# Kernel tuning notes

Hardware: AMD Instinct MI355X
Metric: run time of the kernel (lower is better)

Reference implementation:

```python
import jax, jax.numpy as jnp
import numpy as np

B, S, D = 2, 2048, 1024
H, DK = 16, 64


def setup_inputs() -> dict:
    key = jax.random.key(0)
    ks = jax.random.split(key, 10)
    scale = D ** -0.5
    x = jax.random.normal(ks[0], (B, S, D), dtype=jnp.float32)
    mask = jax.random.randint(ks[1], (B, S), 0, 2) > 0  # True = masked positions
    Wq = jax.random.normal(ks[2], (D, H * DK), dtype=jnp.float32) * scale
    Wk = jax.random.normal(ks[3], (D, H * DK), dtype=jnp.float32) * scale
    Wv = jax.random.normal(ks[4], (D, H * DK), dtype=jnp.float32) * scale
    Wo = jax.random.normal(ks[5], (H * DK, D), dtype=jnp.float32) * scale
    bq = jnp.zeros((H * DK,), jnp.float32)
    bk = jnp.zeros((H * DK,), jnp.float32)
    bv = jnp.zeros((H * DK,), jnp.float32)
    bo = jnp.zeros((D,), jnp.float32)
    return {"x": x, "mask": mask, "Wq": Wq, "bq": bq, "Wk": Wk, "bk": bk,
            "Wv": Wv, "bv": bv, "Wo": Wo, "bo": bo}


def reference(x, mask, Wq, bq, Wk, bk, Wv, bv, Wo, bo):
    b, s, _ = x.shape
    # Linear + activation (dropout is identity at eval)
    q = jax.nn.relu(x @ Wq + bq).reshape(b, s, H, DK)
    k = jax.nn.relu(x @ Wk + bk).reshape(b, s, H, DK)
    v = jax.nn.relu(x @ Wv + bv).reshape(b, s, H, DK)
    # scores: [B, H, Sq, Sk]
    attn = jnp.einsum("bqhd,bkhd->bhqk", q, k) * (DK ** -0.5)
    # NOTE: original uses masked_fill(mask, 1e-9) BEFORE softmax (not -inf)
    attn = jnp.where(mask[:, None, None, :], jnp.float32(1e-9), attn)
    attn = jax.nn.softmax(attn, axis=-1)
    out = jnp.einsum("bhqk,bkhd->bqhd", attn, v).reshape(b, s, H * DK)
    return jax.nn.relu(out @ Wo + bo)
```

## Files before the change

kernel.cpp:

```cpp
#include <hip/hip_runtime.h>
#include <stdint.h>

typedef __attribute__((ext_vector_type(8))) short short8;
typedef __attribute__((ext_vector_type(4))) short short4b;
typedef __attribute__((ext_vector_type(4))) float f32x4;
typedef __attribute__((ext_vector_type(4))) unsigned short ushort4_t;

#define MFMA16(a, b, c) __builtin_amdgcn_mfma_f32_16x16x32_bf16((a), (b), (c), 0, 0, 0)

#if defined(__HIP_DEVICE_COMPILE__)
  #if __has_builtin(__builtin_amdgcn_mfma_f32_16x16x16bf16_1k)
    #define MFMA16K16(a, b, c) __builtin_amdgcn_mfma_f32_16x16x16bf16_1k((a), (b), (c), 0, 0, 0)
  #else
    #define MFMA16K16(a, b, c) __builtin_amdgcn_mfma_f32_16x16x16_bf16((a), (b), (c), 0, 0, 0)
  #endif
#else
  #define MFMA16K16(a, b, c) (c)
#endif

#define SCL_F (0.125f * 1.44269504f)

__device__ __forceinline__ float b2f(unsigned short u) {
    union { unsigned u; float f; } c; c.u = ((unsigned)u) << 16; return c.f;
}
__device__ __forceinline__ unsigned short f2b(float f) {
    union { float f; unsigned u; } c; c.f = f;
    unsigned r = c.u + 0x7FFF + ((c.u >> 16) & 1);
    return (unsigned short)(r >> 16);
}
__device__ __forceinline__ unsigned f_as_u(float f) {
    union { float f; unsigned u; } c; c.f = f; return c.u;
}

__device__ __forceinline__ void g2lds16(const unsigned short* g, unsigned lds_byte_off) {
    __builtin_amdgcn_global_load_lds(
        (const __attribute__((address_space(1))) void*)(uintptr_t)g,
        (__attribute__((address_space(3))) void*)(uintptr_t)lds_byte_off,
        16, 0, 0);
}

__global__ void detect_dtype(const unsigned short* __restrict__ x, int* __restrict__ flag) {
    __shared__ int cnt;
    if (threadIdx.x == 0) cnt = 0;
    __syncthreads();
    int insane = 0;
    #pragma unroll
    for (int j = 0; j < 4; ++j) {
        unsigned short u = x[threadIdx.x * 4 + j];
        int e = (u >> 7) & 0xFF;
        if ((e >= 1 && e <= 90) || e >= 165) insane++;
    }
    atomicAdd(&cnt, insane);
    __syncthreads();
    if (threadIdx.x == 0) *flag = (cnt > 128) ? 1 : 0;
}

__global__ __launch_bounds__(256) void convtrans_k(const void* __restrict__ s0, const void* __restrict__ s1,
                                                   const void* __restrict__ s2, const void* __restrict__ s3,
                                                   const void* __restrict__ b0, const void* __restrict__ b1,
                                                   const void* __restrict__ b2, const void* __restrict__ b3s,
                                                   const void* __restrict__ xsrc,
                                                   unsigned short* __restrict__ xdst,
                                                   unsigned short* __restrict__ dstBase,
                                                   unsigned short* __restrict__ dstB3,
                                                   unsigned short* __restrict__ dstBo,
                                                   const int* __restrict__ flag) {
    const int z = blockIdx.z;
    if (z >= 5) {
        if (!*flag) return;
        const int slice = z - 5;
        const size_t i0 = (size_t)slice * 524288 + (blockIdx.y * 16 + blockIdx.x) * 2048 + threadIdx.x * 8;
        const float* s = (const float*)xsrc;
        float4 f0 = *(const float4*)&s[i0];
        float4 f1 = *(const float4*)&s[i0 + 4];
        unsigned short* t = &xdst[i0];
        t[0] = f2b(f0.x); t[1] = f2b(f0.y); t[2] = f2b(f0.z); t[3] = f2b(f0.w);
        t[4] = f2b(f1.x); t[5] = f2b(f1.y); t[6] = f2b(f1.z); t[7] = f2b(f1.w);
        return;
    }
    if (z == 4) {
        if (blockIdx.y != 0 || blockIdx.x >= 4) return;
        const int w = blockIdx.x;
        const void* src = (w == 0) ? b0 : (w == 1) ? b1 : (w == 2) ? b2 : b3s;
        const float bscl = (w == 0) ? SCL_F : 1.0f;
        #pragma unroll
        for (int j = 0; j < 4; ++j) {
            const int i = threadIdx.x * 4 + j;
            float fv = (*flag) ? ((const float*)src)[i] : b2f(((const unsigned short*)src)[i]);
            unsigned short v = f2b(fv * bscl);
            if (w < 3) dstB3[w * 1024 + i] = v;
            else dstBo[i] = v;
        }
        return;
    }
    __shared__ __align__(16) unsigned short tile[64 * 72];
    const void* src = (z == 0) ? s0 : (z == 1) ? s1 : (z == 2) ? s2 : s3;
    unsigned short* dst = dstBase + (size_t)z * 1024 * 1024;
    const float wscl = (z == 0) ? SCL_F : 1.0f;
    const int tid = threadIdx.x;
    const int r0 = blockIdx.y * 64, c0 = blockIdx.x * 64;
    const int rb = tid >> 3, c = (tid & 7) * 8;
    if (*flag) {
        const float* s = (const float*)src;
        #pragma unroll
        for (int it = 0; it < 2; ++it) {
            int rr = it * 32 + rb;
            float4 f0 = *(const float4*)&s[(size_t)(r0 + rr) * 1024 + c0 + c];
            float4 f1 = *(const float4*)&s[(size_t)(r0 + rr) * 1024 + c0 + c + 4];
            unsigned short* t = &tile[rr * 72 + c];
            t[0] = f2b(f0.x * wscl); t[1] = f2b(f0.y * wscl); t[2] = f2b(f0.z * wscl); t[3] = f2b(f0.w * wscl);
            t[4] = f2b(f1.x * wscl); t[5] = f2b(f1.y * wscl); t[6] = f2b(f1.z * wscl); t[7] = f2b(f1.w * wscl);
        }
    } else if (z == 0) {
        const unsigned short* s = (const unsigned short*)src;
        #pragma unroll
        for (int it = 0; it < 2; ++it) {
            int rr = it * 32 + rb;
            union { short8 v; unsigned short u[8]; } in;
            in.v = *(const short8*)&s[(size_t)(r0 + rr) * 1024 + c0 + c];
            unsigned short* t = &tile[rr * 72 + c];
            #pragma unroll
            for (int j = 0; j < 8; ++j) t[j] = f2b(b2f(in.u[j]) * SCL_F);
        }
    } else {
        const unsigned short* s = (const unsigned short*)src;
        #pragma unroll
        for (int it = 0; it < 2; ++it) {
            int rr = it * 32 + rb;
            *(short8*)&tile[rr * 72 + c] = *(const short8*)&s[(size_t)(r0 + rr) * 1024 + c0 + c];
        }
    }
    __syncthreads();
    #pragma unroll
    for (int it = 0; it < 2; ++it) {
        int n = it * 32 + rb, k8 = c;
        union { short8 s; unsigned short u[8]; } tmp;
        #pragma unroll
        for (int j = 0; j < 8; ++j) tmp.u[j] = tile[(k8 + j) * 72 + n];
        *(short8*)&dst[(size_t)(c0 + n) * 1024 + r0 + k8] = tmp.s;
    }
}

__global__ __launch_bounds__(256) void mask_k(unsigned short* __restrict__ qkv,
                                              const int* __restrict__ mask) {
    const int row = blockIdx.x * 2 + (threadIdx.x >> 7);
    const int col = (threadIdx.x & 127) * 8;
    if (mask[row]) {
        const short8 z = {0, 0, 0, 0, 0, 0, 0, 0};
        *(short8*)&qkv[(size_t)row * 3072 + 1024 + col] = z;
    }
}

__global__ __launch_bounds__(256) void gemm_bias_relu(const unsigned short* __restrict__ A,
                                                      const void* __restrict__ Araw,
                                                      const unsigned short* __restrict__ BT,
                                                      const unsigned short* __restrict__ bias,
                                                      void* __restrict__ C,
                                                      unsigned short* __restrict__ VtG,
                                                      const int* __restrict__ flag,
                                                      int M, int N, int K, int mode) {
    __shared__ __align__(16) unsigned short As[128 * 32];
    __shared__ __align__(16) unsigned short Bs[128 * 32];
    const int tid = threadIdx.x;
    const int wave = tid >> 6, lane = tid & 63;
    const int quad = lane >> 4, l16 = lane & 15;
    const int wm = wave >> 1, wn = wave & 1;
    const int m0 = blockIdx.y * 128, n0 = blockIdx.x * 128;

    const unsigned short* Ause = (Araw != nullptr && *flag == 0) ? (const unsigned short*)Araw : A;

    f32x4 acc[4][4];
    #pragma unroll
    for (int i = 0; i < 4; i++)
        #pragma unroll
        for (int j = 0; j < 4; j++) acc[i][j] = (f32x4){0.f, 0.f, 0.f, 0.f};

    const int srow = wave * 32 + (lane >> 2);
    const int sc8  = (lane & 3) * 8;
    const unsigned short* gA0 = Ause + (size_t)(m0 + srow) * K + sc8;
    const unsigned short* gA1 = gA0 + (size_t)16 * K;
    const unsigned short* gB0 = BT + (size_t)(n0 + srow) * K + sc8;
    const unsigned short* gB1 = gB0 + (size_t)16 * K;
    const unsigned ldsA = (unsigned)(uintptr_t)&As[0] + wave * 2048;
    const unsigned ldsB = (unsigned)(uintptr_t)&Bs[0] + wave * 2048;

    for (int k0 = 0; k0 < K; k0 += 32) {
        __syncthreads();
        g2lds16(gA0 + k0, ldsA);
        g2lds16(gA1 + k0, ldsA + 1024);
        g2lds16(gB0 + k0, ldsB);
        g2lds16(gB1 + k0, ldsB + 1024);
        __syncthreads();
        short8 af[4], bf[4];
        #pragma unroll
        for (int i = 0; i < 4; i++) af[i] = *(const short8*)&As[(wm * 64 + i * 16 + l16) * 32 + quad * 8];
        #pragma unroll
        for (int j = 0; j < 4; j++) bf[j] = *(const short8*)&Bs[(wn * 64 + j * 16 + l16) * 32 + quad * 8];
        #pragma unroll
        for (int i = 0; i < 4; i++)
            #pragma unroll
            for (int j = 0; j < 4; j++)
                acc[i][j] = MFMA16(af[i], bf[j], acc[i][j]);
    }

    if (mode == 2 && n0 >= 2048) {
        #pragma unroll
        for (int j = 0; j < 4; j++) {
            const int col = n0 + wn * 64 + j * 16 + l16;
            const int h  = (col - 2048) >> 6;
            const int dk = (col - 2048) & 63;
            const float bj = b2f(bias[col]);
            #pragma unroll
            for (int i = 0; i < 4; i++) {
                const int rowb = m0 + wm * 64 + i * 16 + quad * 4;
                const int bb = rowb >> 11;
                const int s0 = rowb & 2047;
                ushort4_t w;
                #pragma unroll
                for (int r = 0; r < 4; r++) {
                    float v = acc[i][j][r] + bj;
                    v = v > 0.f ? v : 0.f;
                    w[r] = f2b(v);
                }
                *(ushort4_t*)&VtG[(size_t)((bb * 16 + h) * 64 + dk) * 2048 + s0] = w;
            }
        }
    } else {
        const int f32out = (mode == 1) && (*flag != 0);
        #pragma unroll
        for (int j = 0; j < 4; j++) {
            const int col = n0 + wn * 64 + j * 16 + l16;
            const float bj = b2f(bias[col]);
            #pragma unroll
            for (int i = 0; i < 4; i++) {
                const int rowb = m0 + wm * 64 + i * 16 + quad * 4;
                #pragma unroll
                for (int r = 0; r < 4; r++) {
                    float v = acc[i][j][r] + bj;
                    v = v > 0.f ? v : 0.f;
                    if (f32out) ((float*)C)[(size_t)(rowb + r) * N + col] = v;
                    else ((unsigned short*)C)[(size_t)(rowb + r) * N + col] = f2b(v);
                }
            }
        }
    }
}

__global__ __launch_bounds__(256) void attn_kernel(const unsigned short* __restrict__ qkv,
                                                   const unsigned short* __restrict__ VtG,
                                                   unsigned short* __restrict__ out) {
    __shared__ __align__(16) unsigned short Ks[64 * 72];
    __shared__ __align__(16) unsigned short Vs[64 * 72];

    const int qt = blockIdx.x, bh = blockIdx.y;
    const int b = bh >> 4, h = bh & 15;
    const int tid = threadIdx.x, wave = tid >> 6, lane = tid & 63;
    const int quad = lane >> 4, l16 = lane & 15;

    const int qrowA = qt * 128 + wave * 16 + l16;
    const unsigned short* qpA = qkv + (size_t)(b * 2048 + qrowA) * 3072 + h * 64;
    const unsigned short* qpB = qpA + (size_t)64 * 3072;
    const short8 qa0 = *(const short8*)(qpA + quad * 8);
    const short8 qa1 = *(const short8*)(qpA + 32 + quad * 8);
    const short8 qb0 = *(const short8*)(qpB + quad * 8);
    const short8 qb1 = *(const short8*)(qpB + 32 + quad * 8);

    f32x4 oA[4], oB[4], sumA, sumB;
    #pragma unroll
    for (int n = 0; n < 4; n++) { oA[n] = (f32x4){0.f,0.f,0.f,0.f}; oB[n] = (f32x4){0.f,0.f,0.f,0.f}; }
    sumA = (f32x4){0.f,0.f,0.f,0.f};
    sumB = (f32x4){0.f,0.f,0.f,0.f};

    const short4b ones = { (short)0x3F80, (short)0x3F80, (short)0x3F80, (short)0x3F80 };

    const int srow = tid >> 2;
    const int scol = (tid & 3) * 16;
    const unsigned short* kg = qkv + (size_t)(b * 2048 + srow) * 3072 + 1024 + h * 64 + scol;
    const unsigned short* vg = VtG + (size_t)(bh * 64 + srow) * 2048 + scol;
    const size_t kstep = (size_t)64 * 3072;
    unsigned short* wK = &Ks[srow * 72 + scol];
    unsigned short* wV = &Vs[srow * 72 + scol];

    for (int kt = 0; kt < 32; ++kt) {
        __syncthreads();
        *(short8*)wK       = *(const short8*)(kg + kt * kstep);
        *(short8*)(wK + 8) = *(const short8*)(kg + kt * kstep + 8);
        *(short8*)wV       = *(const short8*)(vg + kt * 64);
        *(short8*)(wV + 8) = *(const short8*)(vg + kt * 64 + 8);
        __syncthreads();

        f32x4 sA[4], sB[4];
        #pragma unroll
        for (int t = 0; t < 4; ++t) {
            const short8 kb0 = *(const short8*)&Ks[(t * 16 + l16) * 72 + quad * 8];
            const short8 kb1 = *(const short8*)&Ks[(t * 16 + l16) * 72 + 32 + quad * 8];
            f32x4 z = (f32x4){0.f, 0.f, 0.f, 0.f};
            sA[t] = MFMA16(kb1, qa1, MFMA16(kb0, qa0, z));
            sB[t] = MFMA16(kb1, qb1, MFMA16(kb0, qb0, z));
        }

        short4b vb[4][4];
        #pragma unroll
        for (int t = 0; t < 4; ++t)
            #pragma unroll
            for (int n = 0; n < 4; ++n)
                vb[t][n] = *(const short4b*)&Vs[(n * 16 + l16) * 72 + t * 16 + quad * 4];

        #pragma unroll
        for (int t = 0; t < 4; ++t) {
            float pA[4], pB[4];
            #pragma unroll
            for (int r = 0; r < 4; ++r) {
                pA[r] = exp2f(sA[t][r]);
                pB[r] = exp2f(sB[t][r]);
            }
            union { unsigned u[2]; short4b s; } fa, fb;
            fa.u[0] = __builtin_amdgcn_perm(f_as_u(pA[1]), f_as_u(pA[0]), 0x07060302u);
            fa.u[1] = __builtin_amdgcn_perm(f_as_u(pA[3]), f_as_u(pA[2]), 0x07060302u);
            fb.u[0] = __builtin_amdgcn_perm(f_as_u(pB[1]), f_as_u(pB[0]), 0x07060302u);
            fb.u[1] = __builtin_amdgcn_perm(f_as_u(pB[3]), f_as_u(pB[2]), 0x07060302u);
            #pragma unroll
            for (int n = 0; n < 4; ++n) {
                oA[n] = MFMA16K16(fa.s, vb[t][n], oA[n]);
                oB[n] = MFMA16K16(fb.s, vb[t][n], oB[n]);
            }
            sumA = MFMA16K16(fa.s, ones, sumA);
            sumB = MFMA16K16(fb.s, ones, sumB);
        }
    }

    float invA[4], invB[4];
    #pragma unroll
    for (int r = 0; r < 4; ++r) { invA[r] = 1.0f / sumA[r]; invB[r] = 1.0f / sumB[r]; }
    #pragma unroll
    for (int n = 0; n < 4; n++)
        #pragma unroll
        for (int r = 0; r < 4; r++) {
            const int row = qt * 128 + wave * 16 + quad * 4 + r;
            out[(size_t)(b * 2048 + row) * 1024 + h * 64 + n * 16 + l16] = f2b(oA[n][r] * invA[r]);
            out[(size_t)(b * 2048 + row + 64) * 1024 + h * 64 + n * 16 + l16] = f2b(oB[n][r] * invB[r]);
        }
}

extern "C" void kernel_launch(void* const* d_in, const int* in_sizes, int n_in,
                              void* d_out, int out_size, void* d_ws, size_t ws_size,
                              hipStream_t stream) {
    const void* x  = d_in[0];
    const int*  mk = (const int*)d_in[1];
    const void* Wq = d_in[2]; const void* bq = d_in[3];
    const void* Wk = d_in[4]; const void* bk = d_in[5];
    const void* Wv = d_in[6]; const void* bv = d_in[7];
    const void* Wo = d_in[8]; const void* bo = d_in[9];

    char* wsb = (char*)d_ws;
    int* flag = (int*)wsb;
    unsigned short* W0 = (unsigned short*)(wsb + 64);

    const size_t M1 = 1024u * 1024u;
    const size_t M4 = 4096u * 1024u;
    unsigned short* xb  = W0;
    unsigned short* WT  = xb + M4;
    unsigned short* WoT = WT + 3 * M1;
    unsigned short* b3  = WoT + M1;
    unsigned short* bob = b3 + 4096;
    unsigned short* qkv = bob + 1024;
    unsigned short* VtG = qkv + (size_t)4096 * 3072;
    unsigned short* abf = xb;

    detect_dtype<<<1, 256, 0, stream>>>((const unsigned short*)x, flag);

    convtrans_k<<<dim3(16, 16, 13), 256, 0, stream>>>(Wq, Wk, Wv, Wo, bq, bk, bv, bo,
                                                      x, xb, WT, b3, bob, flag);

    gemm_bias_relu<<<dim3(24, 32), 256, 0, stream>>>(xb, x, WT, b3, qkv, VtG, flag,
                                                     4096, 3072, 1024, 2);
    mask_k<<<2048, 256, 0, stream>>>(qkv, mk);
    attn_kernel<<<dim3(16, 32), 256, 0, stream>>>(qkv, VtG, abf);
    gemm_bias_relu<<<dim3(8, 32), 256, 0, stream>>>(abf, nullptr, WoT, bob, d_out, VtG, flag,
                                                    4096, 1024, 1024, 1);
}
```

Before: 233.7 us.

## Split attention key range across two blocks and combine partial results

The attention kernel gains a z grid dimension that splits the 2048 keys into two halves. Each block writes unnormalized partial outputs in bf16 plus per-row softmax sums, reusing the free x buffer and the now-unused V columns of qkv. A new combine kernel adds the two partials and divides by the summed denominators. This doubles the number of attention blocks to improve CU occupancy and latency hiding, at the cost of an extra launch, extra memory traffic and bf16 rounding of the unnormalized partials.

```diff
diff --git a/kernel.cpp b/kernel.cpp
--- a/kernel.cpp
+++ b/kernel.cpp
@@ -248,11 +248,13 @@
 
 __global__ __launch_bounds__(256) void attn_kernel(const unsigned short* __restrict__ qkv,
                                                    const unsigned short* __restrict__ VtG,
-                                                   unsigned short* __restrict__ out) {
+                                                   unsigned short* __restrict__ P0,
+                                                   unsigned short* __restrict__ P1,
+                                                   float* __restrict__ S) {
     __shared__ __align__(16) unsigned short Ks[64 * 72];
     __shared__ __align__(16) unsigned short Vs[64 * 72];
 
-    const int qt = blockIdx.x, bh = blockIdx.y;
+    const int qt = blockIdx.x, bh = blockIdx.y, z = blockIdx.z;
     const int b = bh >> 4, h = bh & 15;
     const int tid = threadIdx.x, wave = tid >> 6, lane = tid & 63;
     const int quad = lane >> 4, l16 = lane & 15;
@@ -275,13 +277,13 @@
 
     const int srow = tid >> 2;
     const int scol = (tid & 3) * 16;
-    const unsigned short* kg = qkv + (size_t)(b * 2048 + srow) * 3072 + 1024 + h * 64 + scol;
-    const unsigned short* vg = VtG + (size_t)(bh * 64 + srow) * 2048 + scol;
+    const unsigned short* kg = qkv + (size_t)(b * 2048 + z * 1024 + srow) * 3072 + 1024 + h * 64 + scol;
+    const unsigned short* vg = VtG + (size_t)(bh * 64 + srow) * 2048 + z * 1024 + scol;
     const size_t kstep = (size_t)64 * 3072;
     unsigned short* wK = &Ks[srow * 72 + scol];
     unsigned short* wV = &Vs[srow * 72 + scol];
 
-    for (int kt = 0; kt < 32; ++kt) {
+    for (int kt = 0; kt < 16; ++kt) {
         __syncthreads();
         *(short8*)wK       = *(const short8*)(kg + kt * kstep);
         *(short8*)(wK + 8) = *(const short8*)(kg + kt * kstep + 8);
@@ -294,9 +296,9 @@
         for (int t = 0; t < 4; ++t) {
             const short8 kb0 = *(const short8*)&Ks[(t * 16 + l16) * 72 + quad * 8];
             const short8 kb1 = *(const short8*)&Ks[(t * 16 + l16) * 72 + 32 + quad * 8];
-            f32x4 z = (f32x4){0.f, 0.f, 0.f, 0.f};
-            sA[t] = MFMA16(kb1, qa1, MFMA16(kb0, qa0, z));
-            sB[t] = MFMA16(kb1, qb1, MFMA16(kb0, qb0, z));
+            f32x4 zz = (f32x4){0.f, 0.f, 0.f, 0.f};
+            sA[t] = MFMA16(kb1, qa1, MFMA16(kb0, qa0, zz));
+            sB[t] = MFMA16(kb1, qb1, MFMA16(kb0, qb0, zz));
         }
 
         short4b vb[4][4];
@@ -329,17 +331,45 @@
         }
     }
 
-    float invA[4], invB[4];
-    #pragma unroll
-    for (int r = 0; r < 4; ++r) { invA[r] = 1.0f / sumA[r]; invB[r] = 1.0f / sumB[r]; }
+    unsigned short* pbase = z ? P1 : P0;
+    const int pstr = z ? 3072 : 1024;
     #pragma unroll
     for (int n = 0; n < 4; n++)
         #pragma unroll
         for (int r = 0; r < 4; r++) {
             const int row = qt * 128 + wave * 16 + quad * 4 + r;
-            out[(size_t)(b * 2048 + row) * 1024 + h * 64 + n * 16 + l16] = f2b(oA[n][r] * invA[r]);
-            out[(size_t)(b * 2048 + row + 64) * 1024 + h * 64 + n * 16 + l16] = f2b(oB[n][r] * invB[r]);
-        }
+            pbase[(size_t)(b * 2048 + row) * pstr + h * 64 + n * 16 + l16] = f2b(oA[n][r]);
+            pbase[(size_t)(b * 2048 + row + 64) * pstr + h * 64 + n * 16 + l16] = f2b(oB[n][r]);
+        }
+    if (l16 == 0) {
+        #pragma unroll
+        for (int r = 0; r < 4; r++) {
+            const int row = qt * 128 + wave * 16 + quad * 4 + r;
+            S[((size_t)z * 4096 + b * 2048 + row) * 16 + h] = sumA[r];
+            S[((size_t)z * 4096 + b * 2048 + row + 64) * 16 + h] = sumB[r];
+        }
+    }
+}
+
+__global__ __launch_bounds__(256) void attn_combine(const unsigned short* __restrict__ P0,
+                                                    const unsigned short* __restrict__ P1,
+                                                    const float* __restrict__ S,
+                                                    unsigned short* __restrict__ out) {
+    const int grow = blockIdx.x;
+    __shared__ float inv[16];
+    if (threadIdx.x < 16)
+        inv[threadIdx.x] = 1.0f / (S[(size_t)grow * 16 + threadIdx.x] +
+                                   S[(size_t)(4096 + grow) * 16 + threadIdx.x]);
+    __syncthreads();
+    const int col = threadIdx.x * 4;
+    const int h = col >> 6;
+    const float iv = inv[h];
+    ushort4_t a = *(const ushort4_t*)&P0[(size_t)grow * 1024 + col];
+    ushort4_t c = *(const ushort4_t*)&P1[(size_t)grow * 3072 + col];
+    ushort4_t w;
+    #pragma unroll
+    for (int r = 0; r < 4; r++) w[r] = f2b((b2f(a[r]) + b2f(c[r])) * iv);
+    *(ushort4_t*)&out[(size_t)grow * 1024 + col] = w;
 }
 
 extern "C" void kernel_launch(void* const* d_in, const int* in_sizes, int n_in,
@@ -365,6 +395,8 @@
     unsigned short* bob = b3 + 4096;
     unsigned short* qkv = bob + 1024;
     unsigned short* VtG = qkv + (size_t)4096 * 3072;
+    float* S = (float*)(VtG + M4);
+    unsigned short* P1  = qkv + 2048;
     unsigned short* abf = xb;
 
     detect_dtype<<<1, 256, 0, stream>>>((const unsigned short*)x, flag);
@@ -375,7 +407,8 @@
     gemm_bias_relu<<<dim3(24, 32), 256, 0, stream>>>(xb, x, WT, b3, qkv, VtG, flag,
                                                      4096, 3072, 1024, 2);
     mask_k<<<2048, 256, 0, stream>>>(qkv, mk);
-    attn_kernel<<<dim3(16, 32), 256, 0, stream>>>(qkv, VtG, abf);
+    attn_kernel<<<dim3(16, 32, 2), 256, 0, stream>>>(qkv, VtG, xb, P1, S);
+    attn_combine<<<4096, 256, 0, stream>>>(xb, P1, S, abf);
     gemm_bias_relu<<<dim3(8, 32), 256, 0, stream>>>(abf, nullptr, WoT, bob, d_out, VtG, flag,
                                                     4096, 1024, 1024, 1);
 }
```

After: 241.9 us. +3.5%, slower.
